# Kernel optimization log

Measured on AMD Instinct MI355X. Metric: run time of the kernel, lower is better.

The kernel has to match this reference:

```python
import jax, jax.numpy as jnp
import numpy as np

TOP_K = 2
B, T, D, H, E = 4, 2048, 1024, 2048, 8


def setup_inputs() -> dict:
    key = jax.random.key(0)
    ks = jax.random.split(key, 5)
    x = jax.random.normal(ks[0], (B, T, D), dtype=jnp.float32)
    # router: nn.Linear(dim, n_exp, bias=True) -> weight [E, D], bias [E]
    router_w = jax.random.normal(ks[1], (E, D), dtype=jnp.float32) * (D ** -0.5)
    router_b = jnp.zeros((E,), dtype=jnp.float32)
    # experts stacked: gate/up weight [E, H, D], down weight [E, D, H] (torch Linear is [out, in])
    w_gate = jax.random.normal(ks[2], (E, H, D), dtype=jnp.float32) * (D ** -0.5)
    w_up = jax.random.normal(ks[3], (E, H, D), dtype=jnp.float32) * (D ** -0.5)
    w_down = jax.random.normal(ks[4], (E, D, H), dtype=jnp.float32) * (H ** -0.5)
    return {"x": x, "router_w": router_w, "router_b": router_b,
            "w_gate": w_gate, "w_up": w_up, "w_down": w_down}


def reference(x, router_w, router_b, w_gate, w_up, w_down):
    b, t, d = x.shape
    n_exp = router_w.shape[0]
    flat = x.reshape(-1, d)                                  # [N, D]
    logits = flat @ router_w.T + router_b                    # [N, E]
    probs = jax.nn.softmax(logits, axis=-1)
    top_vals, top_idx = jax.lax.top_k(probs, TOP_K)          # [N, K]
    top_vals = top_vals / (jnp.sum(top_vals, axis=-1, keepdims=True) + 1e-9)
    # dense combine weights [N, E]: scatter normalized top-k probs to expert slots
    comb = jnp.sum(jax.nn.one_hot(top_idx, n_exp, dtype=flat.dtype) * top_vals[..., None], axis=1)
    # run every expert on every token (jit-friendly dense form of gather/scatter loop)
    g = jnp.einsum('nd,ehd->enh', flat, w_gate)              # [E, N, H]
    u = jnp.einsum('nd,ehd->enh', flat, w_up)
    h = jax.nn.silu(g) * u                                   # SwiGLU
    e_out = jnp.einsum('enh,edh->end', h, w_down)            # [E, N, D]
    out = jnp.einsum('ne,end->nd', comb, e_out)              # weighted combine
    return out.reshape(b, t, d)
```

## Files before the change

kernel.cpp:

```cpp
#include <hip/hip_runtime.h>
#include <hip/hip_bf16.h>
#include <stdint.h>


#define N_TOK 8192
#define D_DIM 1024
#define H_DIM 2048
#define N_EXP 8
#define N_ASSIGN (N_TOK * 2)
#define BM 128
#define BN 128
#define BK 64

typedef __attribute__((ext_vector_type(8))) short short8;
typedef __attribute__((ext_vector_type(4))) float f32x4;

__device__ __forceinline__ unsigned short f2bf(float f) {
  union { float f; unsigned int u; } v; v.f = f;
  unsigned int r = v.u + 0x7fffu + ((v.u >> 16) & 1u);
  return (unsigned short)(r >> 16);
}
__device__ __forceinline__ float bf2f(unsigned short u) {
  union { float f; unsigned int u; } v; v.u = ((unsigned int)u) << 16; return v.f;
}
__device__ __forceinline__ short8 pack8(float4 a, float4 b) {
  short8 o;
  o[0] = (short)f2bf(a.x); o[1] = (short)f2bf(a.y);
  o[2] = (short)f2bf(a.z); o[3] = (short)f2bf(a.w);
  o[4] = (short)f2bf(b.x); o[5] = (short)f2bf(b.y);
  o[6] = (short)f2bf(b.z); o[7] = (short)f2bf(b.w);
  return o;
}
__device__ __forceinline__ void gload_lds16(const void* g, void* l) {
  __builtin_amdgcn_global_load_lds((const __attribute__((address_space(1))) void*)g,
                                   (__attribute__((address_space(3))) void*)l, 16, 0, 0);
}

__global__ __launch_bounds__(256) void router_prep_kernel(
    const float* __restrict__ x, const float* __restrict__ rw,
    const float* __restrict__ rb,
    const float* __restrict__ wg, const float* __restrict__ wu,
    unsigned short* __restrict__ xb, unsigned short* __restrict__ wgu,
    int2* __restrict__ tiidx, float2* __restrict__ tiw) {
  int b = blockIdx.x;
  int tid = threadIdx.x;
  if (b >= 2048) {
    int idx = b - 2048;
    int up = idx >> 13;
    size_t i = (((size_t)(idx & 8191)) * 256 + tid) * 8;
    const float* src = up ? wu : wg;
    float4 a = *(const float4*)(src + i);
    float4 c = *(const float4*)(src + i + 4);
    int j = (int)(i >> 10);
    int e = j >> 11;
    int jj = j & (H_DIM - 1);
    int n = ((jj >> 4) << 5) + (up ? 16 : 0) + (jj & 15);
    size_t di = (((size_t)(e << 12) + n) << 10) + (i & 1023);
    *(short8*)(wgu + di) = pack8(a, c);
    return;
  }

  __shared__ float sw[N_EXP][D_DIM];
  for (int i = tid * 4; i < N_EXP * D_DIM; i += 1024)
    *(float4*)&sw[0][i] = *(const float4*)(rw + i);
  __syncthreads();

  int wave = tid >> 6, lane = tid & 63;
  int t = b * 4 + wave;
  const float2* xr = (const float2*)(x + (size_t)t * D_DIM);
  float2 xs[8];
#pragma unroll
  for (int j = 0; j < 8; j++) xs[j] = xr[lane + 64 * j];
  unsigned int* xbo = (unsigned int*)(xb + (size_t)t * D_DIM);
#pragma unroll
  for (int j = 0; j < 8; j++) {
    unsigned int pk = ((unsigned int)f2bf(xs[j].y) << 16) | (unsigned int)f2bf(xs[j].x);
    xbo[lane + 64 * j] = pk;
  }

  float logit[N_EXP];
#pragma unroll
  for (int e = 0; e < N_EXP; e++) {
    float acc = 0.f;
    const float2* swe = (const float2*)sw[e];
#pragma unroll
    for (int j = 0; j < 8; j++) {
      float2 w2 = swe[lane + 64 * j];
      acc += xs[j].x * w2.x + xs[j].y * w2.y;
    }
#pragma unroll
    for (int off = 32; off; off >>= 1) acc += __shfl_xor(acc, off);
    logit[e] = acc + rb[e];
  }
  if (lane == 0) {
    float m = logit[0];
#pragma unroll
    for (int e = 1; e < N_EXP; e++) m = fmaxf(m, logit[e]);
    float p[N_EXP], S = 0.f;
#pragma unroll
    for (int e = 0; e < N_EXP; e++) { p[e] = expf(logit[e] - m); S += p[e]; }
#pragma unroll
    for (int e = 0; e < N_EXP; e++) p[e] /= S;
    int i1 = 0; float v1 = p[0];
#pragma unroll
    for (int e = 1; e < N_EXP; e++) if (p[e] > v1) { v1 = p[e]; i1 = e; }
    int i2 = -1; float v2 = -1.f;
#pragma unroll
    for (int e = 0; e < N_EXP; e++) if (e != i1 && p[e] > v2) { v2 = p[e]; i2 = e; }
    float inv = 1.f / (v1 + v2 + 1e-9f);
    tiidx[t] = make_int2(i1, i2);
    tiw[t] = make_float2(v1 * inv, v2 * inv);
  }
}

__global__ __launch_bounds__(256) void plan_kernel(
    const int2* __restrict__ tiidx, int* __restrict__ cnt,
    int* __restrict__ off, int* __restrict__ assign, int2* __restrict__ trows) {
  __shared__ int sh[256][N_EXP + 1];
  __shared__ int soff[N_EXP];
  int tid = threadIdx.x;
  int t0 = tid * 32;

#pragma unroll
  for (int e = 0; e < N_EXP; e++) sh[tid][e] = 0;
  for (int i = 0; i < 32; i++) {
    int2 te = tiidx[t0 + i];
    sh[tid][te.x]++;
    sh[tid][te.y]++;
  }
  int oc[N_EXP];
#pragma unroll
  for (int e = 0; e < N_EXP; e++) oc[e] = sh[tid][e];
  __syncthreads();

  for (int s = 1; s < 256; s <<= 1) {
    int v[N_EXP];
#pragma unroll
    for (int e = 0; e < N_EXP; e++) v[e] = (tid >= s) ? sh[tid - s][e] : 0;
    __syncthreads();
#pragma unroll
    for (int e = 0; e < N_EXP; e++) sh[tid][e] += v[e];
    __syncthreads();
  }

  int ex[N_EXP];
#pragma unroll
  for (int e = 0; e < N_EXP; e++) ex[e] = sh[tid][e] - oc[e];
  if (tid == 0) {
    int a = 0;
    for (int e = 0; e < N_EXP; e++) {
      int tot = sh[255][e];
      soff[e] = a; off[e] = a; cnt[e] = tot; a += tot;
    }
    off[N_EXP] = a;
  }
  __syncthreads();
#pragma unroll
  for (int e = 0; e < N_EXP; e++) sh[tid][e] = ex[e];
  __syncthreads();

  for (int i = 0; i < 32; i++) {
    int t = t0 + i;
    int2 te = tiidx[t];
    int r1 = soff[te.x] + sh[tid][te.x]++;
    int r2 = soff[te.y] + sh[tid][te.y]++;
    assign[r1] = t;
    assign[r2] = t;
    trows[t] = make_int2(r1, r2);
  }
}

__global__ __launch_bounds__(512, 2) void gemm_gateup(
    const unsigned short* __restrict__ xb,
    const unsigned short* __restrict__ wgu,
    const float* __restrict__ wd,
    unsigned short* __restrict__ wdb,
    const int* __restrict__ cnt, const int* __restrict__ off,
    const int* __restrict__ assign,
    unsigned short* __restrict__ hbuf) {
  int tid = threadIdx.x;
  if (blockIdx.z == 8) {
    size_t b0 = ((size_t)(blockIdx.x + 16 * blockIdx.y)) * 4096;
#pragma unroll
    for (int it = 0; it < 8; it++) {
      size_t i = (b0 + (size_t)it * 512 + tid) * 8;
      float4 a = *(const float4*)(wd + i);
      float4 c = *(const float4*)(wd + i + 4);
      *(short8*)(wdb + i) = pack8(a, c);
    }
    return;
  }
  int e = blockIdx.z;
  int nrows = cnt[e];
  int row0 = blockIdx.y * 256;
  if (row0 >= nrows) return;
  int col0 = blockIdx.x * 256;
  int base = off[e];

  __shared__ unsigned short sA[2][256][BK];
  __shared__ unsigned short sB[2][256][BK];

  int srow = tid >> 3;
  int dst8 = (tid & 7) * 8;
  int src8 = ((tid & 7) ^ (srow & 7)) * 8;

  const unsigned short* asrc[4];
  const unsigned short* bsrc[4];
#pragma unroll
  for (int i = 0; i < 4; i++) {
    int r = row0 + srow + 64 * i;
    int tok = (r < nrows) ? assign[base + r] : assign[base];
    asrc[i] = xb + (size_t)tok * D_DIM + src8;
    int wrow = (e << 12) + col0 + srow + 64 * i;
    bsrc[i] = wgu + (size_t)wrow * D_DIM + src8;
  }

  int wid = tid >> 6;
  int wr = wid >> 2;
  int wc = wid & 3;
  int lane = tid & 63;
  int fr = lane & 15;
  int fq = lane >> 4;
  int fk = fq * 8;
  int rx = (fr & 7) * 8;

  f32x4 acc[8][4];
#pragma unroll
  for (int a = 0; a < 8; a++)
#pragma unroll
    for (int b = 0; b < 4; b++) acc[a][b] = (f32x4){0.f, 0.f, 0.f, 0.f};

#define STAGE(bf, k0)                                                       \
  _Pragma("unroll")                                                         \
  for (int i = 0; i < 4; i++) {                                             \
    gload_lds16(asrc[i] + (k0), &sA[bf][srow + 64 * i][dst8]);              \
    gload_lds16(bsrc[i] + (k0), &sB[bf][srow + 64 * i][dst8]);              \
  }
#define COMPUTE(bf)                                                         \
  _Pragma("unroll")                                                         \
  for (int ks = 0; ks < 2; ks++) {                                          \
    short8 af[8], bq[4];                                                    \
    int c = (ks * 32 + fk) ^ rx;                                            \
    _Pragma("unroll")                                                       \
    for (int mb = 0; mb < 8; mb++)                                          \
      af[mb] = *(const short8*)&sA[bf][wr * 128 + mb * 16 + fr][c];         \
    _Pragma("unroll")                                                       \
    for (int nb = 0; nb < 4; nb++)                                          \
      bq[nb] = *(const short8*)&sB[bf][wc * 64 + nb * 16 + fr][c];          \
    _Pragma("unroll")                                                       \
    for (int mb = 0; mb < 8; mb++)                                          \
      _Pragma("unroll")                                                     \
      for (int nb = 0; nb < 4; nb++)                                        \
        acc[mb][nb] = __builtin_amdgcn_mfma_f32_16x16x32_bf16(              \
            af[mb], bq[nb], acc[mb][nb], 0, 0, 0);                          \
  }

  STAGE(0, 0);
  for (int t = 0; t < 15; ++t) {
    STAGE((t + 1) & 1, (t + 1) * BK);
    asm volatile("s_waitcnt vmcnt(8)" ::: "memory");
    __builtin_amdgcn_sched_barrier(0);
    __builtin_amdgcn_s_barrier();
    __builtin_amdgcn_sched_barrier(0);
    __builtin_amdgcn_s_setprio(1);
    COMPUTE(t & 1);
    __builtin_amdgcn_s_setprio(0);
    __builtin_amdgcn_sched_barrier(0);
    __builtin_amdgcn_s_barrier();
    __builtin_amdgcn_sched_barrier(0);
  }
  asm volatile("s_waitcnt vmcnt(0)" ::: "memory");
  __builtin_amdgcn_sched_barrier(0);
  __builtin_amdgcn_s_barrier();
  __builtin_amdgcn_sched_barrier(0);
  COMPUTE(1);
#undef STAGE
#undef COMPUTE

  int rowlim = nrows - row0;
#pragma unroll
  for (int mb = 0; mb < 8; mb++)
#pragma unroll
    for (int r = 0; r < 4; r++) {
      int lrow = wr * 128 + mb * 16 + fq * 4 + r;
      if (lrow < rowlim) {
        size_t hrow = (size_t)(base + row0 + lrow);
#pragma unroll
        for (int nbp = 0; nbp < 2; nbp++) {
          float g = acc[mb][2 * nbp][r], u = acc[mb][2 * nbp + 1][r];
          float hv = g / (1.f + __expf(-g)) * u;
          int hcol = (col0 >> 1) + wc * 32 + nbp * 16 + fr;
          hbuf[hrow * H_DIM + hcol] = f2bf(hv);
        }
      }
    }
}

__global__ __launch_bounds__(256) void gemm_down(
    const unsigned short* __restrict__ hbuf,
    const unsigned short* __restrict__ wd,
    const int* __restrict__ cnt, const int* __restrict__ off,
    unsigned short* __restrict__ eo) {
  int e = blockIdx.z;
  int nrows = cnt[e];
  int row0 = blockIdx.y * BM;
  if (row0 >= nrows) return;
  int col0 = blockIdx.x * BN;
  int base = off[e];

  __shared__ unsigned short sA[2][BM][BK];
  __shared__ unsigned short sB[2][BN][BK];

  int tid = threadIdx.x;
  int srow = tid >> 3;
  int dst8 = (tid & 7) * 8;
  int src8 = ((tid & 7) ^ (srow & 7)) * 8;

  const unsigned short* asrc[4];
  const unsigned short* bsrc[4];
#pragma unroll
  for (int i = 0; i < 4; i++) {
    int r = row0 + srow + 32 * i;
    int hrow = base + ((r < nrows) ? r : 0);
    asrc[i] = hbuf + (size_t)hrow * H_DIM + src8;
    int wrow = e * D_DIM + col0 + srow + 32 * i;
    bsrc[i] = wd + (size_t)wrow * H_DIM + src8;
  }

  int wr = (tid >> 7) & 1, wc = (tid >> 6) & 1;
  int lane = tid & 63;
  int fr = lane & 15;
  int fk = (lane >> 4) * 8;
  int rx = (fr & 7) * 8;

  f32x4 acc[4][4];
#pragma unroll
  for (int a = 0; a < 4; a++)
#pragma unroll
    for (int b = 0; b < 4; b++) acc[a][b] = (f32x4){0.f, 0.f, 0.f, 0.f};

#define STAGE(bf, k0)                                                       \
  _Pragma("unroll")                                                         \
  for (int i = 0; i < 4; i++) {                                             \
    gload_lds16(asrc[i] + (k0), &sA[bf][srow + 32 * i][dst8]);              \
    gload_lds16(bsrc[i] + (k0), &sB[bf][srow + 32 * i][dst8]);              \
  }
#define COMPUTE(bf)                                                         \
  _Pragma("unroll")                                                         \
  for (int ks = 0; ks < 2; ks++) {                                          \
    short8 af[4], bq[4];                                                    \
    int c = (ks * 32 + fk) ^ rx;                                            \
    _Pragma("unroll")                                                       \
    for (int mb = 0; mb < 4; mb++)                                          \
      af[mb] = *(const short8*)&sA[bf][wr * 64 + mb * 16 + fr][c];          \
    _Pragma("unroll")                                                       \
    for (int nb = 0; nb < 4; nb++)                                          \
      bq[nb] = *(const short8*)&sB[bf][wc * 64 + nb * 16 + fr][c];          \
    _Pragma("unroll")                                                       \
    for (int mb = 0; mb < 4; mb++)                                          \
      _Pragma("unroll")                                                     \
      for (int nb = 0; nb < 4; nb++)                                        \
        acc[mb][nb] = __builtin_amdgcn_mfma_f32_16x16x32_bf16(              \
            af[mb], bq[nb], acc[mb][nb], 0, 0, 0);                          \
  }

  STAGE(0, 0);
  __syncthreads();
  for (int k0 = 0; k0 < H_DIM - 128; k0 += 128) {
    STAGE(1, k0 + 64);  COMPUTE(0); __syncthreads();
    STAGE(0, k0 + 128); COMPUTE(1); __syncthreads();
  }
  STAGE(1, H_DIM - 64); COMPUTE(0); __syncthreads();
  COMPUTE(1);
#undef STAGE
#undef COMPUTE

  int rowlim = nrows - row0;
#pragma unroll
  for (int mb = 0; mb < 4; mb++)
#pragma unroll
    for (int r = 0; r < 4; r++) {
      int lrow = wr * 64 + mb * 16 + (lane >> 4) * 4 + r;
      if (lrow < rowlim) {
        size_t orow = (size_t)(base + row0 + lrow);
#pragma unroll
        for (int nb = 0; nb < 4; nb++)
          eo[orow * D_DIM + col0 + wc * 64 + nb * 16 + (lane & 15)] = f2bf(acc[mb][nb][r]);
      }
    }
}

__global__ __launch_bounds__(256) void combine_kernel(
    const unsigned short* __restrict__ eo, const int2* __restrict__ trows,
    const float2* __restrict__ tiw, float* __restrict__ out) {
  int t = blockIdx.x * 2 + (threadIdx.x >> 7);
  int l = threadIdx.x & 127;
  int c = l * 8;
  int2 r = trows[t];
  float2 w = tiw[t];
  short8 a = *(const short8*)&eo[(size_t)r.x * D_DIM + c];
  short8 b = *(const short8*)&eo[(size_t)r.y * D_DIM + c];
  float4 o0, o1;
  o0.x = w.x * bf2f((unsigned short)a[0]) + w.y * bf2f((unsigned short)b[0]);
  o0.y = w.x * bf2f((unsigned short)a[1]) + w.y * bf2f((unsigned short)b[1]);
  o0.z = w.x * bf2f((unsigned short)a[2]) + w.y * bf2f((unsigned short)b[2]);
  o0.w = w.x * bf2f((unsigned short)a[3]) + w.y * bf2f((unsigned short)b[3]);
  o1.x = w.x * bf2f((unsigned short)a[4]) + w.y * bf2f((unsigned short)b[4]);
  o1.y = w.x * bf2f((unsigned short)a[5]) + w.y * bf2f((unsigned short)b[5]);
  o1.z = w.x * bf2f((unsigned short)a[6]) + w.y * bf2f((unsigned short)b[6]);
  o1.w = w.x * bf2f((unsigned short)a[7]) + w.y * bf2f((unsigned short)b[7]);
  *(float4*)&out[(size_t)t * D_DIM + c] = o0;
  *(float4*)&out[(size_t)t * D_DIM + c + 4] = o1;
}

extern "C" void kernel_launch(void* const* d_in, const int* in_sizes, int n_in,
                              void* d_out, int out_size, void* d_ws, size_t ws_size,
                              hipStream_t stream) {
  const float* x  = (const float*)d_in[0];
  const float* rw = (const float*)d_in[1];
  const float* rb = (const float*)d_in[2];
  const float* wg = (const float*)d_in[3];
  const float* wu = (const float*)d_in[4];
  const float* wd = (const float*)d_in[5];
  float* out = (float*)d_out;

  char* ws = (char*)d_ws;
  size_t o = 0;
  auto alloc = [&](size_t b) { char* p = ws + o; o += (b + 255) & ~(size_t)255; return p; };
  unsigned short* xb  = (unsigned short*)alloc((size_t)N_TOK * D_DIM * 2);
  unsigned short* wgu = (unsigned short*)alloc((size_t)N_EXP * 4096 * D_DIM * 2);
  unsigned short* wdb = (unsigned short*)alloc((size_t)N_EXP * D_DIM * H_DIM * 2);
  unsigned short* hb  = (unsigned short*)alloc((size_t)N_ASSIGN * H_DIM * 2);
  unsigned short* eob = (unsigned short*)alloc((size_t)N_ASSIGN * D_DIM * 2);
  int*    assign = (int*)alloc(N_ASSIGN * 4);
  int2*   tiidx  = (int2*)alloc(N_TOK * 8);
  float2* tiw    = (float2*)alloc(N_TOK * 8);
  int2*   trows  = (int2*)alloc(N_TOK * 8);
  int*    cnt    = (int*)alloc(64);
  int*    off    = (int*)alloc(64);

  router_prep_kernel<<<2048 + 16384, 256, 0, stream>>>(
      x, rw, rb, wg, wu, xb, wgu, tiidx, tiw);
  plan_kernel<<<1, 256, 0, stream>>>(tiidx, cnt, off, assign, trows);
  gemm_gateup<<<dim3(4096 / 256, 32, N_EXP + 1), 512, 0, stream>>>(
      xb, wgu, wd, wdb, cnt, off, assign, hb);
  gemm_down<<<dim3(D_DIM / BN, N_TOK / BM, N_EXP), 256, 0, stream>>>(
      hb, wdb, cnt, off, eob);
  combine_kernel<<<N_TOK / 2, 256, 0, stream>>>(eob, trows, tiw, out);
}
```

Baseline: 368.2 us.

## Triple-buffer LDS pipelines and retile both expert GEMMs to 128x256

Both grouped GEMMs move to 128x256 tiles with 512 threads and a three-stage LDS ring. Each step issues its global-to-LDS prefetch two stages ahead, and one barrier per iteration replaces the previous two. The gate/up kernel halves its M tile to give more blocks per expert, and the down kernel doubles its block size and N tile. The weight-conversion slice inside gate/up is remapped to fit the larger grid, which adds LDS pressure and more blocks that may exit early.

```diff
diff --git a/kernel.cpp b/kernel.cpp
--- a/kernel.cpp
+++ b/kernel.cpp
@@ -8,9 +8,6 @@
 #define H_DIM 2048
 #define N_EXP 8
 #define N_ASSIGN (N_TOK * 2)
-#define BM 128
-#define BN 128
-#define BK 64
 
 typedef __attribute__((ext_vector_type(8))) short short8;
 typedef __attribute__((ext_vector_type(4))) float f32x4;
@@ -180,10 +177,10 @@
     unsigned short* __restrict__ hbuf) {
   int tid = threadIdx.x;
   if (blockIdx.z == 8) {
-    size_t b0 = ((size_t)(blockIdx.x + 16 * blockIdx.y)) * 4096;
-#pragma unroll
-    for (int it = 0; it < 8; it++) {
-      size_t i = (b0 + (size_t)it * 512 + tid) * 8;
+    size_t b0 = ((size_t)(blockIdx.x + 16 * blockIdx.y)) * 16384;
+#pragma unroll
+    for (int it = 0; it < 4; it++) {
+      size_t i = b0 + ((size_t)it * 512 + tid) * 8;
       float4 a = *(const float4*)(wd + i);
       float4 c = *(const float4*)(wd + i + 4);
       *(short8*)(wdb + i) = pack8(a, c);
@@ -192,25 +189,28 @@
   }
   int e = blockIdx.z;
   int nrows = cnt[e];
-  int row0 = blockIdx.y * 256;
+  int row0 = blockIdx.y * 128;
   if (row0 >= nrows) return;
   int col0 = blockIdx.x * 256;
   int base = off[e];
 
-  __shared__ unsigned short sA[2][256][BK];
-  __shared__ unsigned short sB[2][256][BK];
+  __shared__ unsigned short sA[3][128][64];
+  __shared__ unsigned short sB[3][256][64];
 
   int srow = tid >> 3;
   int dst8 = (tid & 7) * 8;
   int src8 = ((tid & 7) ^ (srow & 7)) * 8;
 
-  const unsigned short* asrc[4];
-  const unsigned short* bsrc[4];
-#pragma unroll
-  for (int i = 0; i < 4; i++) {
+  const unsigned short* asrc[2];
+#pragma unroll
+  for (int i = 0; i < 2; i++) {
     int r = row0 + srow + 64 * i;
     int tok = (r < nrows) ? assign[base + r] : assign[base];
     asrc[i] = xb + (size_t)tok * D_DIM + src8;
+  }
+  const unsigned short* bsrc[4];
+#pragma unroll
+  for (int i = 0; i < 4; i++) {
     int wrow = (e << 12) + col0 + srow + 64 * i;
     bsrc[i] = wgu + (size_t)wrow * D_DIM + src8;
   }
@@ -224,65 +224,66 @@
   int fk = fq * 8;
   int rx = (fr & 7) * 8;
 
-  f32x4 acc[8][4];
-#pragma unroll
-  for (int a = 0; a < 8; a++)
+  f32x4 acc[4][4];
+#pragma unroll
+  for (int a = 0; a < 4; a++)
 #pragma unroll
     for (int b = 0; b < 4; b++) acc[a][b] = (f32x4){0.f, 0.f, 0.f, 0.f};
 
 #define STAGE(bf, k0)                                                       \
-  _Pragma("unroll")                                                         \
-  for (int i = 0; i < 4; i++) {                                             \
-    gload_lds16(asrc[i] + (k0), &sA[bf][srow + 64 * i][dst8]);              \
-    gload_lds16(bsrc[i] + (k0), &sB[bf][srow + 64 * i][dst8]);              \
+  {                                                                         \
+    _Pragma("unroll")                                                       \
+    for (int i = 0; i < 2; i++)                                             \
+      gload_lds16(asrc[i] + (k0), &sA[bf][srow + 64 * i][dst8]);            \
+    _Pragma("unroll")                                                       \
+    for (int i = 0; i < 4; i++)                                             \
+      gload_lds16(bsrc[i] + (k0), &sB[bf][srow + 64 * i][dst8]);            \
   }
 #define COMPUTE(bf)                                                         \
   _Pragma("unroll")                                                         \
   for (int ks = 0; ks < 2; ks++) {                                          \
-    short8 af[8], bq[4];                                                    \
+    short8 af[4], bq[4];                                                    \
     int c = (ks * 32 + fk) ^ rx;                                            \
     _Pragma("unroll")                                                       \
-    for (int mb = 0; mb < 8; mb++)                                          \
-      af[mb] = *(const short8*)&sA[bf][wr * 128 + mb * 16 + fr][c];         \
+    for (int mb = 0; mb < 4; mb++)                                          \
+      af[mb] = *(const short8*)&sA[bf][wr * 64 + mb * 16 + fr][c];          \
     _Pragma("unroll")                                                       \
     for (int nb = 0; nb < 4; nb++)                                          \
       bq[nb] = *(const short8*)&sB[bf][wc * 64 + nb * 16 + fr][c];          \
-    _Pragma("unroll")                                                       \
-    for (int mb = 0; mb < 8; mb++)                                          \
+    __builtin_amdgcn_s_setprio(1);                                          \
+    _Pragma("unroll")                                                       \
+    for (int mb = 0; mb < 4; mb++)                                          \
       _Pragma("unroll")                                                     \
       for (int nb = 0; nb < 4; nb++)                                        \
         acc[mb][nb] = __builtin_amdgcn_mfma_f32_16x16x32_bf16(              \
             af[mb], bq[nb], acc[mb][nb], 0, 0, 0);                          \
+    __builtin_amdgcn_s_setprio(0);                                          \
   }
 
   STAGE(0, 0);
+  STAGE(1, 64);
   for (int t = 0; t < 15; ++t) {
-    STAGE((t + 1) & 1, (t + 1) * BK);
-    asm volatile("s_waitcnt vmcnt(8)" ::: "memory");
+    asm volatile("s_waitcnt vmcnt(6)" ::: "memory");
     __builtin_amdgcn_sched_barrier(0);
     __builtin_amdgcn_s_barrier();
     __builtin_amdgcn_sched_barrier(0);
-    __builtin_amdgcn_s_setprio(1);
-    COMPUTE(t & 1);
-    __builtin_amdgcn_s_setprio(0);
-    __builtin_amdgcn_sched_barrier(0);
-    __builtin_amdgcn_s_barrier();
-    __builtin_amdgcn_sched_barrier(0);
+    if (t < 14) { int nb3 = (t + 2) % 3; STAGE(nb3, (t + 2) * 64); }
+    COMPUTE(t % 3);
   }
   asm volatile("s_waitcnt vmcnt(0)" ::: "memory");
   __builtin_amdgcn_sched_barrier(0);
   __builtin_amdgcn_s_barrier();
   __builtin_amdgcn_sched_barrier(0);
-  COMPUTE(1);
+  COMPUTE(0);
 #undef STAGE
 #undef COMPUTE
 
   int rowlim = nrows - row0;
 #pragma unroll
-  for (int mb = 0; mb < 8; mb++)
+  for (int mb = 0; mb < 4; mb++)
 #pragma unroll
     for (int r = 0; r < 4; r++) {
-      int lrow = wr * 128 + mb * 16 + fq * 4 + r;
+      int lrow = wr * 64 + mb * 16 + fq * 4 + r;
       if (lrow < rowlim) {
         size_t hrow = (size_t)(base + row0 + lrow);
 #pragma unroll
@@ -296,41 +297,47 @@
     }
 }
 
-__global__ __launch_bounds__(256) void gemm_down(
+__global__ __launch_bounds__(512, 2) void gemm_down(
     const unsigned short* __restrict__ hbuf,
     const unsigned short* __restrict__ wd,
     const int* __restrict__ cnt, const int* __restrict__ off,
     unsigned short* __restrict__ eo) {
   int e = blockIdx.z;
   int nrows = cnt[e];
-  int row0 = blockIdx.y * BM;
+  int row0 = blockIdx.y * 128;
   if (row0 >= nrows) return;
-  int col0 = blockIdx.x * BN;
+  int col0 = blockIdx.x * 256;
   int base = off[e];
 
-  __shared__ unsigned short sA[2][BM][BK];
-  __shared__ unsigned short sB[2][BN][BK];
+  __shared__ unsigned short sA[3][128][64];
+  __shared__ unsigned short sB[3][256][64];
 
   int tid = threadIdx.x;
   int srow = tid >> 3;
   int dst8 = (tid & 7) * 8;
   int src8 = ((tid & 7) ^ (srow & 7)) * 8;
 
-  const unsigned short* asrc[4];
-  const unsigned short* bsrc[4];
-#pragma unroll
-  for (int i = 0; i < 4; i++) {
-    int r = row0 + srow + 32 * i;
+  const unsigned short* asrc[2];
+#pragma unroll
+  for (int i = 0; i < 2; i++) {
+    int r = row0 + srow + 64 * i;
     int hrow = base + ((r < nrows) ? r : 0);
     asrc[i] = hbuf + (size_t)hrow * H_DIM + src8;
-    int wrow = e * D_DIM + col0 + srow + 32 * i;
+  }
+  const unsigned short* bsrc[4];
+#pragma unroll
+  for (int i = 0; i < 4; i++) {
+    int wrow = e * D_DIM + col0 + srow + 64 * i;
     bsrc[i] = wd + (size_t)wrow * H_DIM + src8;
   }
 
-  int wr = (tid >> 7) & 1, wc = (tid >> 6) & 1;
+  int wid = tid >> 6;
+  int wr = wid >> 2;
+  int wc = wid & 3;
   int lane = tid & 63;
   int fr = lane & 15;
-  int fk = (lane >> 4) * 8;
+  int fq = lane >> 4;
+  int fk = fq * 8;
   int rx = (fr & 7) * 8;
 
   f32x4 acc[4][4];
@@ -340,10 +347,13 @@
     for (int b = 0; b < 4; b++) acc[a][b] = (f32x4){0.f, 0.f, 0.f, 0.f};
 
 #define STAGE(bf, k0)                                                       \
-  _Pragma("unroll")                                                         \
-  for (int i = 0; i < 4; i++) {                                             \
-    gload_lds16(asrc[i] + (k0), &sA[bf][srow + 32 * i][dst8]);              \
-    gload_lds16(bsrc[i] + (k0), &sB[bf][srow + 32 * i][dst8]);              \
+  {                                                                         \
+    _Pragma("unroll")                                                       \
+    for (int i = 0; i < 2; i++)                                             \
+      gload_lds16(asrc[i] + (k0), &sA[bf][srow + 64 * i][dst8]);            \
+    _Pragma("unroll")                                                       \
+    for (int i = 0; i < 4; i++)                                             \
+      gload_lds16(bsrc[i] + (k0), &sB[bf][srow + 64 * i][dst8]);            \
   }
 #define COMPUTE(bf)                                                         \
   _Pragma("unroll")                                                         \
@@ -356,21 +366,30 @@
     _Pragma("unroll")                                                       \
     for (int nb = 0; nb < 4; nb++)                                          \
       bq[nb] = *(const short8*)&sB[bf][wc * 64 + nb * 16 + fr][c];          \
+    __builtin_amdgcn_s_setprio(1);                                          \
     _Pragma("unroll")                                                       \
     for (int mb = 0; mb < 4; mb++)                                          \
       _Pragma("unroll")                                                     \
       for (int nb = 0; nb < 4; nb++)                                        \
         acc[mb][nb] = __builtin_amdgcn_mfma_f32_16x16x32_bf16(              \
             af[mb], bq[nb], acc[mb][nb], 0, 0, 0);                          \
+    __builtin_amdgcn_s_setprio(0);                                          \
   }
 
   STAGE(0, 0);
-  __syncthreads();
-  for (int k0 = 0; k0 < H_DIM - 128; k0 += 128) {
-    STAGE(1, k0 + 64);  COMPUTE(0); __syncthreads();
-    STAGE(0, k0 + 128); COMPUTE(1); __syncthreads();
-  }
-  STAGE(1, H_DIM - 64); COMPUTE(0); __syncthreads();
+  STAGE(1, 64);
+  for (int t = 0; t < 31; ++t) {
+    asm volatile("s_waitcnt vmcnt(6)" ::: "memory");
+    __builtin_amdgcn_sched_barrier(0);
+    __builtin_amdgcn_s_barrier();
+    __builtin_amdgcn_sched_barrier(0);
+    if (t < 30) { int nb3 = (t + 2) % 3; STAGE(nb3, (t + 2) * 64); }
+    COMPUTE(t % 3);
+  }
+  asm volatile("s_waitcnt vmcnt(0)" ::: "memory");
+  __builtin_amdgcn_sched_barrier(0);
+  __builtin_amdgcn_s_barrier();
+  __builtin_amdgcn_sched_barrier(0);
   COMPUTE(1);
 #undef STAGE
 #undef COMPUTE
@@ -380,12 +399,12 @@
   for (int mb = 0; mb < 4; mb++)
 #pragma unroll
     for (int r = 0; r < 4; r++) {
-      int lrow = wr * 64 + mb * 16 + (lane >> 4) * 4 + r;
+      int lrow = wr * 64 + mb * 16 + fq * 4 + r;
       if (lrow < rowlim) {
         size_t orow = (size_t)(base + row0 + lrow);
 #pragma unroll
         for (int nb = 0; nb < 4; nb++)
-          eo[orow * D_DIM + col0 + wc * 64 + nb * 16 + (lane & 15)] = f2bf(acc[mb][nb][r]);
+          eo[orow * D_DIM + col0 + wc * 64 + nb * 16 + fr] = f2bf(acc[mb][nb][r]);
       }
     }
 }
@@ -442,9 +461,9 @@
   router_prep_kernel<<<2048 + 16384, 256, 0, stream>>>(
       x, rw, rb, wg, wu, xb, wgu, tiidx, tiw);
   plan_kernel<<<1, 256, 0, stream>>>(tiidx, cnt, off, assign, trows);
-  gemm_gateup<<<dim3(4096 / 256, 32, N_EXP + 1), 512, 0, stream>>>(
+  gemm_gateup<<<dim3(4096 / 256, N_TOK / 128, N_EXP + 1), 512, 0, stream>>>(
       xb, wgu, wd, wdb, cnt, off, assign, hb);
-  gemm_down<<<dim3(D_DIM / BN, N_TOK / BM, N_EXP), 256, 0, stream>>>(
+  gemm_down<<<dim3(D_DIM / 256, N_TOK / 128, N_EXP), 512, 0, stream>>>(
       hb, wdb, cnt, off, eob);
   combine_kernel<<<N_TOK / 2, 256, 0, stream>>>(eob, trows, tiw, out);
 }
```

Result: slower. 428.8 us (+16.5%).
